# Optimization experiments

Hardware: AMD Instinct MI355X
Metric: run time of the kernel (lower is better)

## Reference

```python
import jax, jax.numpy as jnp
import numpy as np

K = 4        # num_kernels
TOPK = 16    # per-row hyperedge sparsification
CHEB_T = 2   # Chebyshev order
ROW_TEMP = 1.0
PI_ITERS = 5  # power-iteration steps


def setup_inputs() -> dict:
    key = jax.random.key(0)
    N, D, D_out = 4096, 256, 256
    ks = jax.random.split(key, 5)
    X = jax.random.normal(ks[0], (N, D), jnp.float32)
    L_k = jax.random.normal(ks[1], (K, D, D), jnp.float32) * 0.02
    alpha = jnp.ones((K,), jnp.float32)
    theta = jax.random.normal(ks[2], (CHEB_T + 1, D), jnp.float32) * 0.02
    rho_raw = jnp.zeros((), jnp.float32)
    proj_w = jax.random.normal(ks[3], (D_out, D), jnp.float32) / np.sqrt(D).astype(np.float32)
    proj_b = jnp.zeros((D_out,), jnp.float32)
    return {"X": X, "L_k": L_k, "alpha": alpha, "theta": theta,
            "rho_raw": rho_raw, "proj_w": proj_w, "proj_b": proj_b}


def reference(X, L_k, alpha, theta, rho_raw, proj_w, proj_b):
    N, D = X.shape
    tau = max(ROW_TEMP, 1e-6)
    # 1) K bilinear kernels: A_k = X L_k X^T / sqrt(D), row-softmax with temp
    A = jnp.einsum('nd,kde,me->knm', X, L_k, X) / jnp.sqrt(jnp.asarray(D, X.dtype))
    H_stack = jax.nn.softmax(A / tau, axis=2)                 # (K, N, N)
    w = jax.nn.softmax(alpha)[:, None, None]
    H_fused = (H_stack * w).sum(0)                            # (N, N)
    # 2) incidence B (N, E=K*N): hyperedge (k,i) holds topk targets of row i of head k
    vals, idx = jax.lax.top_k(H_stack, TOPK)                  # (K, N, TOPK)
    vals = vals / (vals.sum(-1, keepdims=True) + 1e-9)
    E = K * N
    cols = jnp.arange(K)[:, None, None] * N + jnp.arange(N)[None, :, None]
    cols = jnp.broadcast_to(cols, (K, N, TOPK)).reshape(-1)
    rows = idx.reshape(-1)
    B = jnp.zeros((N, E), X.dtype).at[rows, cols].set(vals.reshape(-1))
    W = jnp.ones((E,), X.dtype)
    # 3) normalized hypergraph Laplacian L = I - Dv^{-1/2} B W De^{-1} B^T Dv^{-1/2}
    De = B.sum(0) + 1e-9                                      # (E,)
    Dv = (B * W[None, :]).sum(1) + 1e-9                       # (N,)
    Dv_is = jnp.sqrt(1.0 / Dv)
    S = (B * (W / De)[None, :]) @ B.T                         # (N, N)
    S_norm = Dv_is[:, None] * S * Dv_is[None, :]
    I = jnp.eye(N, dtype=X.dtype)
    L = I - S_norm
    # 4) lambda_max via power iteration on detached L (constant w.r.t. grads)
    Ld = jax.lax.stop_gradient(L)
    v = jax.random.normal(jax.random.key(1), (N, 1), X.dtype)
    v = v / (jnp.linalg.norm(v) + 1e-9)
    for _ in range(PI_ITERS):
        v = Ld @ v
        v = v / (jnp.linalg.norm(v) + 1e-9)
    lam = jnp.clip((v.T @ (Ld @ v)).squeeze(), 1e-3, None)
    lam = jax.lax.stop_gradient(lam)
    L_tilde = (2.0 / lam) * L - I
    # Chebyshev recursion: sum_t T_t(L_tilde) X * theta_t, then ELU
    T0 = X
    out = T0 * theta[0][None, :]
    T1 = L_tilde @ X
    out = out + T1 * theta[1][None, :]
    for t in range(2, CHEB_T + 1):
        T2 = 2.0 * (L_tilde @ T1) - T0
        out = out + T2 * theta[t][None, :]
        T0, T1 = T1, T2
    Z_spec = jax.nn.elu(out)
    # 5) residual blend with kernel diffusion
    Z_kern = H_fused @ X
    rho = jax.nn.sigmoid(rho_raw)
    Z_mix = rho * Z_spec + (1.0 - rho) * Z_kern
    # 6) final projection
    return Z_mix @ proj_w.T + proj_b
```

## Files before the change

kernel.cpp:

```cpp
#include <hip/hip_runtime.h>

typedef unsigned short u16;
typedef unsigned long long u64;
typedef _Float16 h16;
typedef __attribute__((ext_vector_type(8))) _Float16 h16x8;
typedef __attribute__((ext_vector_type(4))) _Float16 h16x4;
typedef __attribute__((ext_vector_type(4))) float f32x4;

__device__ __forceinline__ float b2f(u16 u) {
  unsigned x = ((unsigned)u) << 16;
  return __uint_as_float(x);
}
__device__ __forceinline__ unsigned fkey(float f) {
  unsigned b = __float_as_uint(f);
  return (b & 0x80000000u) ? ~b : (b | 0x80000000u);
}
__device__ __forceinline__ float unfkey(unsigned u) {
  unsigned b = (u & 0x80000000u) ? (u ^ 0x80000000u) : ~u;
  return __uint_as_float(b);
}
__device__ __forceinline__ f32x4 mfma16(h16x8 a, h16x8 b, f32x4 c) {
  return __builtin_amdgcn_mfma_f32_16x16x32_f16(a, b, c, 0, 0, 0);
}
__device__ __forceinline__ void gl_lds16(const void* g, void* l) {
  __builtin_amdgcn_global_load_lds(
      (const __attribute__((address_space(1))) unsigned*)g,
      (__attribute__((address_space(3))) unsigned*)l, 16, 0, 0);
}
__device__ __forceinline__ u64 wave_max_u64(u64 k) {
#pragma unroll
  for (int off = 32; off; off >>= 1) {
    u64 o = __shfl_xor(k, off);
    if (o > k) k = o;
  }
  return k;
}
__device__ __forceinline__ float cvt_in(const void* p, int i, int f) {
  return f ? ((const float*)p)[i] : b2f(((const u16*)p)[i]);
}

__device__ __forceinline__ int detect_f32_local(const u16* __restrict__ X) {
  __shared__ int dcnt;
  if (threadIdx.x == 0) dcnt = 0;
  __syncthreads();
  int sane = 0;
  for (int j = threadIdx.x; j < 4096; j += blockDim.x) {
    u16 u = X[j * 2];
    int e = (u >> 7) & 0xff;
    if (u == 0 || (e >= 112 && e <= 142)) sane++;
  }
  atomicAdd(&dcnt, sane);
  __syncthreads();
  return (dcnt < 3072) ? 1 : 0;
}

__global__ __launch_bounds__(256) void split_input3(
    const void* __restrict__ in, h16* __restrict__ hi, h16* __restrict__ lo,
    float* __restrict__ f32out, int n) {
  int f = detect_f32_local((const u16*)in);
  int stride = gridDim.x * 256;
  for (int i = blockIdx.x * 256 + threadIdx.x; i < n; i += stride) {
    float x = cvt_in(in, i, f);
    h16 h = (h16)x;
    hi[i] = h;
    lo[i] = (h16)(x - (float)h);
    if (f32out) f32out[i] = x;
  }
}

__global__ __launch_bounds__(256) void split_LW(
    const void* __restrict__ Xin, const void* __restrict__ Lin,
    h16* __restrict__ Lhi, h16* __restrict__ Llo, const void* __restrict__ Win,
    h16* __restrict__ Whi, h16* __restrict__ Wlo) {
  int f = detect_f32_local((const u16*)Xin);
  int tid = threadIdx.x;
  if (blockIdx.x < 256) {
#pragma unroll
    for (int j = 0; j < 4; ++j) {
      int i = blockIdx.x * 1024 + j * 256 + tid;
      float x = cvt_in(Lin, i, f);
      h16 h = (h16)x;
      Lhi[i] = h;
      Llo[i] = (h16)(x - (float)h);
    }
  } else {
    int b = blockIdx.x - 256;
#pragma unroll
    for (int j = 0; j < 4; ++j) {
      int i = b * 1024 + j * 256 + tid;
      float x = cvt_in(Win, i, f);
      h16 h = (h16)x;
      Whi[i] = h;
      Wlo[i] = (h16)(x - (float)h);
    }
  }
}

__global__ __launch_bounds__(1024) void prep_small(
    const void* __restrict__ Xin, const void* __restrict__ theta,
    const void* __restrict__ bpin, const void* __restrict__ alpha,
    const void* __restrict__ rho_raw, float* __restrict__ thetaf,
    float* __restrict__ biasf, float* __restrict__ scal) {
  int f = detect_f32_local((const u16*)Xin);
  int tid = threadIdx.x;
  if (tid < 768)
    thetaf[tid] = cvt_in(theta, tid, f);
  else if (tid < 1024)
    biasf[tid - 768] = cvt_in(bpin, tid - 768, f);
  if (tid == 0) {
    float a[4], e[4], m = -1e30f, s = 0.f;
    for (int i = 0; i < 4; ++i) {
      a[i] = cvt_in(alpha, i, f);
      m = fmaxf(m, a[i]);
    }
    for (int i = 0; i < 4; ++i) { e[i] = expf(a[i] - m); s += e[i]; }
    for (int i = 0; i < 4; ++i) scal[i] = e[i] / s;
    float rr = cvt_in(rho_raw, 0, f);
    scal[4] = 1.f / (1.f + expf(-rr));
  }
}

template <bool BIAS, bool SPLITOUT>
__global__ __launch_bounds__(256) void gemm3_nt(
    const h16* __restrict__ Ah, const h16* __restrict__ Al,
    const h16* __restrict__ Bh, const h16* __restrict__ Bl,
    float* __restrict__ C, h16* __restrict__ Yh, h16* __restrict__ Yl,
    const float* __restrict__ bias, float alpha, int M, int Nc, int Kd,
    long batchA, long batchB, long batchC) {
  const h16* Abh = Ah + (size_t)blockIdx.z * batchA;
  const h16* Abl = Al + (size_t)blockIdx.z * batchA;
  const h16* Bbh = Bh + (size_t)blockIdx.z * batchB;
  const h16* Bbl = Bl + (size_t)blockIdx.z * batchB;
  int bn = blockIdx.x, bm = blockIdx.y;
  int tid = threadIdx.x;
  int wid = tid >> 6, lane = tid & 63;
  __shared__ h16 Ash[64 * 40], Asl[64 * 40], Bsh[64 * 40], Bsl[64 * 40];
  f32x4 acc00 = {}, acc01 = {}, acc10 = {}, acc11 = {};
  int lr = tid >> 2;
  int lc = (tid & 3) << 3;
  size_t aoff = (size_t)(bm * 64 + lr) * Kd + lc;
  size_t boff = (size_t)(bn * 64 + lr) * Kd + lc;
  int wm = (wid & 1) * 32, wn = (wid >> 1) * 32;
  int fr = lane & 15;
  int fc = (lane >> 4) << 3;
  for (int k0 = 0; k0 < Kd; k0 += 32) {
    uint4 avh = *(const uint4*)(Abh + aoff + k0);
    uint4 avl = *(const uint4*)(Abl + aoff + k0);
    uint4 bvh = *(const uint4*)(Bbh + boff + k0);
    uint4 bvl = *(const uint4*)(Bbl + boff + k0);
    __syncthreads();
    *(uint4*)(Ash + lr * 40 + lc) = avh;
    *(uint4*)(Asl + lr * 40 + lc) = avl;
    *(uint4*)(Bsh + lr * 40 + lc) = bvh;
    *(uint4*)(Bsl + lr * 40 + lc) = bvl;
    __syncthreads();
    h16x8 a0h = *(const h16x8*)(Ash + (wm + fr) * 40 + fc);
    h16x8 a1h = *(const h16x8*)(Ash + (wm + 16 + fr) * 40 + fc);
    h16x8 b0h = *(const h16x8*)(Bsh + (wn + fr) * 40 + fc);
    h16x8 b1h = *(const h16x8*)(Bsh + (wn + 16 + fr) * 40 + fc);
    h16x8 a0l = *(const h16x8*)(Asl + (wm + fr) * 40 + fc);
    h16x8 a1l = *(const h16x8*)(Asl + (wm + 16 + fr) * 40 + fc);
    h16x8 b0l = *(const h16x8*)(Bsl + (wn + fr) * 40 + fc);
    h16x8 b1l = *(const h16x8*)(Bsl + (wn + 16 + fr) * 40 + fc);
    acc00 = mfma16(a0h, b0h, acc00);
    acc01 = mfma16(a0h, b1h, acc01);
    acc10 = mfma16(a1h, b0h, acc10);
    acc11 = mfma16(a1h, b1h, acc11);
    acc00 = mfma16(a0h, b0l, acc00);
    acc01 = mfma16(a0h, b1l, acc01);
    acc10 = mfma16(a1h, b0l, acc10);
    acc11 = mfma16(a1h, b1l, acc11);
    acc00 = mfma16(a0l, b0h, acc00);
    acc01 = mfma16(a0l, b1h, acc01);
    acc10 = mfma16(a1l, b0h, acc10);
    acc11 = mfma16(a1l, b1h, acc11);
  }
  int crow = (lane >> 4) << 2;
  int ccol = lane & 15;
  f32x4 accs[2][2] = {{acc00, acc01}, {acc10, acc11}};
#pragma unroll
  for (int i = 0; i < 2; ++i)
#pragma unroll
    for (int j = 0; j < 2; ++j) {
      int r0 = bm * 64 + wm + 16 * i + crow;
      int c0 = bn * 64 + wn + 16 * j + ccol;
#pragma unroll
      for (int rg = 0; rg < 4; ++rg) {
        size_t off = (size_t)(r0 + rg) * Nc + c0;
        float v = accs[i][j][rg] * alpha;
        if constexpr (SPLITOUT) {
          h16* Yhb = Yh + (size_t)blockIdx.z * batchC;
          h16* Ylb = Yl + (size_t)blockIdx.z * batchC;
          h16 hh = (h16)v;
          Yhb[off] = hh;
          Ylb[off] = (h16)(v - (float)hh);
        } else {
          if constexpr (BIAS) v += bias[c0];
          float* Cb = C + (size_t)blockIdx.z * batchC;
          Cb[off] = v;
        }
      }
    }
}

__global__ __launch_bounds__(256) void gemm3_big(
    const h16* __restrict__ Ah, const h16* __restrict__ Al,
    const h16* __restrict__ Bh, const h16* __restrict__ Bl,
    float* __restrict__ C, float alpha, int M, int Nc, int Kd) {
  __shared__ h16 sAh[128 * 32], sAl[128 * 32], sBh[128 * 32], sBl[128 * 32];
  int tid = threadIdx.x, wid = tid >> 6, lane = tid & 63;
  int bm = blockIdx.y, bn = blockIdx.x;
  int srow = 32 * wid + (lane >> 2);
  int scnk = lane & 3;
  int fr = lane & 15, fcc = lane >> 4;
  f32x4 acc[4][4] = {};
  const h16* gA[2] = {Ah, Al};
  const h16* gB[2] = {Bh, Bl};
  h16* sA[2] = {sAh, sAl};
  h16* sB[2] = {sBh, sBl};
  int wm = (wid & 1) * 64, wn = (wid >> 1) * 64;
  for (int k0 = 0; k0 < Kd; k0 += 32) {
    __syncthreads();
#pragma unroll
    for (int h = 0; h < 2; ++h) {
      int r = srow + 16 * h;
      int cs = scnk ^ ((r >> 1) & 3);
      size_t goffA = (size_t)(bm * 128 + r) * Kd + k0 + cs * 8;
      size_t goffB = (size_t)(bn * 128 + r) * Kd + k0 + cs * 8;
      int loff = (32 * wid + 16 * h) * 32;
#pragma unroll
      for (int p = 0; p < 2; ++p) {
        gl_lds16(gA[p] + goffA, sA[p] + loff);
        gl_lds16(gB[p] + goffB, sB[p] + loff);
      }
    }
    __syncthreads();
    h16x8 fa[2][4], fb[2][4];
#pragma unroll
    for (int i = 0; i < 4; ++i) {
      int ra = wm + 16 * i + fr;
      int ca = (fcc ^ ((ra >> 1) & 3)) * 8;
      fa[0][i] = *(const h16x8*)(sAh + ra * 32 + ca);
      fa[1][i] = *(const h16x8*)(sAl + ra * 32 + ca);
      int rb = wn + 16 * i + fr;
      int cb = (fcc ^ ((rb >> 1) & 3)) * 8;
      fb[0][i] = *(const h16x8*)(sBh + rb * 32 + cb);
      fb[1][i] = *(const h16x8*)(sBl + rb * 32 + cb);
    }
#pragma unroll
    for (int i = 0; i < 4; ++i)
#pragma unroll
      for (int j = 0; j < 4; ++j) {
        acc[i][j] = mfma16(fa[0][i], fb[0][j], acc[i][j]);
        acc[i][j] = mfma16(fa[0][i], fb[1][j], acc[i][j]);
        acc[i][j] = mfma16(fa[1][i], fb[0][j], acc[i][j]);
      }
  }
  int crow = (lane >> 4) << 2, ccol = lane & 15;
#pragma unroll
  for (int i = 0; i < 4; ++i)
#pragma unroll
    for (int j = 0; j < 4; ++j) {
      int r0 = bm * 128 + wm + 16 * i + crow;
      int c0 = bn * 128 + wn + 16 * j + ccol;
#pragma unroll
      for (int rg = 0; rg < 4; ++rg)
        C[(size_t)(r0 + rg) * Nc + c0] = acc[i][j][rg] * alpha;
    }
}

__global__ __launch_bounds__(256) void gemm_ks4(
    const h16* __restrict__ Eall, const h16* __restrict__ B,
    float* __restrict__ Cpart) {
  __shared__ h16 sA[2][64 * 32];
  __shared__ h16 sB[2][256 * 32];
  int tid = threadIdx.x, wid = tid >> 6, lane = tid & 63;
  int bm = blockIdx.x, zz = blockIdx.y;
  int head = zz >> 2, kz = zz & 3;
  const h16* A =
      Eall + (size_t)head * 4096 * 4096 + (size_t)(bm * 64) * 4096 + kz * 1024;
  const h16* Bb = B + kz * 1024;
  int r16 = lane >> 2;
  int scnk = lane & 3;
  int fr = lane & 15, fcc = lane >> 4;
  int wn = wid * 64;
  f32x4 acc[4][4] = {};

  int rA = 16 * wid + r16;
  size_t gA = (size_t)rA * 4096 + scnk * 8;
  size_t gB[4];
  int dB[4];
  int dA = rA * 32 + ((scnk ^ ((rA >> 1) & 3)) << 3);
#pragma unroll
  for (int p = 0; p < 4; ++p) {
    int rB = 64 * p + 16 * wid + r16;
    gB[p] = (size_t)rB * 4096 + scnk * 8;
    dB[p] = rB * 32 + ((scnk ^ ((rB >> 1) & 3)) << 3);
  }

  uint4 rgA, rgB0, rgB1, rgB2, rgB3;
  auto gload = [&](int k0) {
    rgA = *(const uint4*)(A + gA + k0);
    rgB0 = *(const uint4*)(Bb + gB[0] + k0);
    rgB1 = *(const uint4*)(Bb + gB[1] + k0);
    rgB2 = *(const uint4*)(Bb + gB[2] + k0);
    rgB3 = *(const uint4*)(Bb + gB[3] + k0);
  };
  auto swrite = [&](int buf) {
    *(uint4*)(&sA[buf][dA]) = rgA;
    *(uint4*)(&sB[buf][dB[0]]) = rgB0;
    *(uint4*)(&sB[buf][dB[1]]) = rgB1;
    *(uint4*)(&sB[buf][dB[2]]) = rgB2;
    *(uint4*)(&sB[buf][dB[3]]) = rgB3;
  };
  auto compute = [&](int buf) {
    h16x8 fa[4], fb[4];
#pragma unroll
    for (int i = 0; i < 4; ++i) {
      int ra = 16 * i + fr;
      int ca = (fcc ^ ((ra >> 1) & 3)) * 8;
      fa[i] = *(const h16x8*)(&sA[buf][ra * 32 + ca]);
      int rb = wn + 16 * i + fr;
      int cb = (fcc ^ ((rb >> 1) & 3)) * 8;
      fb[i] = *(const h16x8*)(&sB[buf][rb * 32 + cb]);
    }
#pragma unroll
    for (int i = 0; i < 4; ++i)
#pragma unroll
      for (int j = 0; j < 4; ++j)
        acc[i][j] = mfma16(fa[i], fb[j], acc[i][j]);
  };

  gload(0);
  swrite(0);
  gload(32);
  __syncthreads();
  for (int t = 0; t < 32; ++t) {
    int cur = t & 1;
    if (t < 31) {
      swrite(cur ^ 1);
      if (t < 30) gload((t + 2) * 32);
    }
    compute(cur);
    __syncthreads();
  }

  float* Cp = Cpart + (size_t)zz * 4096 * 256;
  int crow = (lane >> 4) << 2, ccol = lane & 15;
#pragma unroll
  for (int i = 0; i < 4; ++i)
#pragma unroll
    for (int j = 0; j < 4; ++j) {
      int r0 = bm * 64 + 16 * i + crow;
      int c0 = wn + 16 * j + ccol;
#pragma unroll
      for (int rg = 0; rg < 4; ++rg)
        Cp[(size_t)(r0 + rg) * 256 + c0] = acc[i][j][rg];
    }
}

__global__ __launch_bounds__(256) void ksred_hist(
    const float* __restrict__ Cpart, const float* __restrict__ scal,
    const float* __restrict__ rowSinv, float* __restrict__ Zk,
    const float* __restrict__ topv, const int* __restrict__ topi,
    int* __restrict__ pCnt, float* __restrict__ pDv,
    float* __restrict__ DeIS) {
  __shared__ int lc[4096];
  __shared__ float ld[4096];
  int tid = threadIdx.x;
  if (blockIdx.x < 1024) {
    int i = (blockIdx.x * 256 + tid) * 4;
    int row = i >> 8;
    float4 out = {0.f, 0.f, 0.f, 0.f};
#pragma unroll
    for (int k = 0; k < 4; ++k) {
      float4 s = {0.f, 0.f, 0.f, 0.f};
#pragma unroll
      for (int z = 0; z < 4; ++z) {
        float4 p =
            *(const float4*)(Cpart + (size_t)(k * 4 + z) * 4096 * 256 + i);
        s.x += p.x; s.y += p.y; s.z += p.z; s.w += p.w;
      }
      float sc = scal[k] * rowSinv[k * 4096 + row];
      out.x += sc * s.x; out.y += sc * s.y;
      out.z += sc * s.z; out.w += sc * s.w;
    }
    *(float4*)(Zk + i) = out;
  } else {
    int b = blockIdx.x - 1024;
    for (int j = tid; j < 4096; j += 256) { lc[j] = 0; ld[j] = 0.f; }
    __syncthreads();
    int base = b * 4096;
#pragma unroll
    for (int j = 0; j < 16; ++j) {
      int t = base + j * 256 + tid;
      atomicAdd(&lc[topi[t]], 1);
      atomicAdd(&ld[topi[t]], topv[t]);
    }
    __syncthreads();
    for (int j = tid; j < 4096; j += 256) {
      pCnt[base + j] = lc[j];
      pDv[base + j] = ld[j];
    }
    int e = b * 256 + tid;
    const float4* p = (const float4*)(topv + ((size_t)e << 4));
    float4 a = p[0], bb = p[1], c = p[2], d = p[3];
    float s = ((a.x + a.y) + (a.z + a.w)) + ((bb.x + bb.y) + (bb.z + bb.w)) +
              ((c.x + c.y) + (c.z + c.w)) + ((d.x + d.y) + (d.z + d.w));
    DeIS[e] = 1.0f / sqrtf(s + 1e-9f);
  }
}

__global__ __launch_bounds__(256) void transpose16(
    const u16* __restrict__ in, u16* __restrict__ out, int rows, int cols) {
  __shared__ u16 t[32][33];
  const u16* ib = in + (size_t)blockIdx.z * rows * cols;
  u16* ob = out + (size_t)blockIdx.z * rows * cols;
  int r0 = blockIdx.x * 32, c0 = blockIdx.y * 32;
  int tx = threadIdx.x & 31, ty = threadIdx.x >> 5;
#pragma unroll
  for (int i = 0; i < 32; i += 8)
    t[ty + i][tx] = ib[(size_t)(r0 + ty + i) * cols + c0 + tx];
  __syncthreads();
#pragma unroll
  for (int i = 0; i < 32; i += 8)
    ob[(size_t)(c0 + ty + i) * rows + r0 + tx] = t[tx][ty + i];
}

__global__ __launch_bounds__(256) void row_softmax_topk(
    const float* __restrict__ A, float* __restrict__ topv,
    int* __restrict__ topi, h16* __restrict__ E, float* __restrict__ rowSinvK,
    int khead) {
  __shared__ u64 candK[4][256];
  __shared__ int candN[4];
  int wid = threadIdx.x >> 6, lane = threadIdx.x & 63;
  int row = blockIdx.x * 4 + wid;
  const float* arow = A + ((size_t)row << 12);
  if (lane == 0) candN[wid] = 0;
  __syncthreads();
  float lm = -INFINITY;
#pragma unroll
  for (int t = 0; t < 16; ++t) {
    float4 v = *(const float4*)(arow + (t << 8) + (lane << 2));
    lm = fmaxf(lm, fmaxf(fmaxf(v.x, v.y), fmaxf(v.z, v.w)));
  }
  float m = lm;
#pragma unroll
  for (int off = 32; off; off >>= 1) m = fmaxf(m, __shfl_xor(m, off));
  u64 lk = ((u64)fkey(lm) << 32) | (unsigned)lane;
  float T = 0.f;
  for (int r = 0; r < 16; ++r) {
    u64 k2 = wave_max_u64(lk);
    if (lk == k2) lk = 0;
    if (r == 15) T = unfkey((unsigned)(k2 >> 32));
  }
  h16* erow = E + ((size_t)row << 12);
  int* cn = &candN[wid];
  u64* ck = candK[wid];
  float s = 0.f;
  for (int t = 0; t < 16; ++t) {
    int c = (t << 8) + (lane << 2);
    float4 v = *(const float4*)(arow + c);
    float e0 = __expf(v.x - m), e1 = __expf(v.y - m);
    float e2 = __expf(v.z - m), e3 = __expf(v.w - m);
    s += (e0 + e1) + (e2 + e3);
    h16x4 hv = {(h16)e0, (h16)e1, (h16)e2, (h16)e3};
    *(h16x4*)(erow + c) = hv;
    if (v.x >= T) {
      int sl = atomicAdd(cn, 1);
      if (sl < 256) ck[sl] = ((u64)fkey(v.x) << 32) | (unsigned)(~(unsigned)c);
    }
    if (v.y >= T) {
      int sl = atomicAdd(cn, 1);
      if (sl < 256) ck[sl] = ((u64)fkey(v.y) << 32) | (unsigned)(~(unsigned)(c + 1));
    }
    if (v.z >= T) {
      int sl = atomicAdd(cn, 1);
      if (sl < 256) ck[sl] = ((u64)fkey(v.z) << 32) | (unsigned)(~(unsigned)(c + 2));
    }
    if (v.w >= T) {
      int sl = atomicAdd(cn, 1);
      if (sl < 256) ck[sl] = ((u64)fkey(v.w) << 32) | (unsigned)(~(unsigned)(c + 3));
    }
  }
#pragma unroll
  for (int off = 32; off; off >>= 1) s += __shfl_xor(s, off);
  if (lane == 0) rowSinvK[row] = 1.f / s;
  __syncthreads();
  int cnt = min(*cn, 256);
  u64 loc[4] = {0ull, 0ull, 0ull, 0ull};
  int nl = 0;
  for (int j = lane; j < cnt; j += 64)
    if (nl < 4) loc[nl++] = ck[j];
#define CSW(a, b)                     \
  {                                   \
    if (loc[b] > loc[a]) {            \
      u64 tt = loc[a];                \
      loc[a] = loc[b];                \
      loc[b] = tt;                    \
    }                                 \
  }
  CSW(0, 1) CSW(2, 3) CSW(0, 2) CSW(1, 3) CSW(1, 2)
#undef CSW
  float myv = 0.f;
  int myi = 0;
  float sum16 = 0.f;
  for (int r = 0; r < 16; ++r) {
    u64 key = loc[0];
    u64 k2 = wave_max_u64(key);
    float wv = unfkey((unsigned)(k2 >> 32));
    int wi = (int)(~(unsigned)(k2 & 0xffffffffu));
    if (key == k2 && key != 0ull) {
      loc[0] = loc[1];
      loc[1] = loc[2];
      loc[2] = loc[3];
      loc[3] = 0ull;
    }
    sum16 += expf(wv - m);
    if (r == lane) { myv = wv; myi = wi; }
  }
  if (lane < 16) {
    size_t o = (((size_t)khead << 12) + row) * 16 + lane;
    topv[o] = expf(myv - m) / (sum16 + 1e-9f * s);
    topi[o] = myi;
  }
}

__global__ __launch_bounds__(256) void col_scan(
    const int* __restrict__ pCnt, const float* __restrict__ pDv,
    int* __restrict__ cnt, float* __restrict__ Dvis,
    int* __restrict__ blockBase, float* __restrict__ v0) {
  int i = blockIdx.x * 256 + threadIdx.x;
  int run = 0;
  float dv = 0.f;
#pragma unroll
  for (int b = 0; b < 64; ++b) {
    blockBase[b * 4096 + i] = run;
    run += pCnt[b * 4096 + i];
    dv += pDv[b * 4096 + i];
  }
  cnt[i] = run;
  Dvis[i] = sqrtf(1.0f / (dv + 1e-9f));
  {
    int tid = i;
    unsigned j = (unsigned)(tid & 2047);
    unsigned x0 = j, x1 = j + 2048u;
    const unsigned ks0 = 0u, ks1 = 1u, ks2 = 0x1BD11BDAu;
#define TF_R(r)                                \
    {                                          \
      x0 += x1;                                \
      x1 = (x1 << (r)) | (x1 >> (32 - (r)));   \
      x1 ^= x0;                                \
    }
    x0 += ks0; x1 += ks1;
    TF_R(13) TF_R(15) TF_R(26) TF_R(6)  x0 += ks1; x1 += ks2 + 1u;
    TF_R(17) TF_R(29) TF_R(16) TF_R(24) x0 += ks2; x1 += ks0 + 2u;
    TF_R(13) TF_R(15) TF_R(26) TF_R(6)  x0 += ks0; x1 += ks1 + 3u;
    TF_R(17) TF_R(29) TF_R(16) TF_R(24) x0 += ks1; x1 += ks2 + 4u;
    TF_R(13) TF_R(15) TF_R(26) TF_R(6)  x0 += ks2; x1 += ks0 + 5u;
#undef TF_R
    unsigned bits = (tid < 2048) ? x0 : x1;
    float u01 = __uint_as_float((bits >> 9) | 0x3f800000u) - 1.0f;
    const float lo = -0.99999994f;
    float u = fmaxf(lo, u01 * 2.0f + lo);
    float w = -log1pf(-u * u);
    float p;
    if (w < 5.0f) {
      float t = w - 2.5f;
      p = 2.81022636e-08f;
      p = 3.43273939e-07f + p * t;
      p = -3.5233877e-06f + p * t;
      p = -4.39150654e-06f + p * t;
      p = 0.00021858087f + p * t;
      p = -0.00125372503f + p * t;
      p = -0.00417768164f + p * t;
      p = 0.246640727f + p * t;
      p = 1.50140941f + p * t;
    } else {
      float t = sqrtf(w) - 3.0f;
      p = -0.000200214257f;
      p = 0.000100950558f + p * t;
      p = 0.00134934322f + p * t;
      p = -0.00367342844f + p * t;
      p = 0.00573950773f + p * t;
      p = -0.0076224613f + p * t;
      p = 0.00943887047f + p * t;
      p = 1.00167406f + p * t;
      p = 2.83297682f + p * t;
    }
    v0[tid] = 1.41421354f * (p * u);
  }
}

__global__ __launch_bounds__(256) void scan_rowptr(const int* __restrict__ cnt,
                                                   int* __restrict__ rowptr) {
  __shared__ int part[256];
  int tid = threadIdx.x;
  int base = tid * 16;
  int loc[16];
  int s = 0;
#pragma unroll
  for (int j = 0; j < 16; ++j) { loc[j] = s; s += cnt[base + j]; }
  part[tid] = s;
  __syncthreads();
  for (int off = 1; off < 256; off <<= 1) {
    int v = (tid >= off) ? part[tid - off] : 0;
    __syncthreads();
    part[tid] += v;
    __syncthreads();
  }
  int pre = (tid == 0) ? 0 : part[tid - 1];
#pragma unroll
  for (int j = 0; j < 16; ++j) rowptr[base + j] = pre + loc[j];
  if (tid == 255) rowptr[4096] = part[255];
}

__global__ __launch_bounds__(256) void csr_fill3(
    const float* __restrict__ topv, const int* __restrict__ topi,
    const float* __restrict__ Dvis, const float* __restrict__ DeIS,
    const int* __restrict__ rowptr, const int* __restrict__ blockBase,
    float* __restrict__ cvals, int* __restrict__ colE,
    float* __restrict__ cvalR) {
  __shared__ int lcur[4096];
  int tid = threadIdx.x, b = blockIdx.x;
  int base = b * 4096;
  for (int j = tid; j < 4096; j += 256)
    lcur[j] = rowptr[j] + blockBase[base + j];
  __syncthreads();
#pragma unroll
  for (int j = 0; j < 16; ++j) {
    int t = base + j * 256 + tid;
    int i = topi[t];
    int e = t >> 4;
    float c = Dvis[i] * topv[t] * DeIS[e];
    cvals[t] = c;
    int slot = atomicAdd(&lcur[i], 1);
    colE[slot] = e;
    cvalR[slot] = c;
  }
}

__global__ __launch_bounds__(256) void spmv_edge(
    const float* __restrict__ cvals, const int* __restrict__ topi,
    const float* __restrict__ v, float* __restrict__ g) {
  int e = blockIdx.x * 256 + threadIdx.x;
  float acc = 0.f;
#pragma unroll
  for (int p = 0; p < 16; ++p)
    acc += cvals[e * 16 + p] * v[topi[e * 16 + p]];
  g[e] = acc;
}

__global__ __launch_bounds__(256) void spmv_row(
    const int* __restrict__ rowptr, const int* __restrict__ colE,
    const float* __restrict__ cvalR, const float* __restrict__ g,
    const float* __restrict__ vin, float* __restrict__ vout) {
  int wid = threadIdx.x >> 6, lane = threadIdx.x & 63;
  int row = blockIdx.x * 4 + wid;
  int s = rowptr[row], e = rowptr[row + 1];
  float acc = 0.f;
  for (int j = s + lane; j < e; j += 64) acc += cvalR[j] * g[colE[j]];
#pragma unroll
  for (int off = 32; off; off >>= 1) acc += __shfl_xor(acc, off);
  if (lane == 0) vout[row] = vin[row] - acc;
}

__global__ __launch_bounds__(256) void pi_dots(const float* __restrict__ w5,
                                               const float* __restrict__ w6,
                                               float* __restrict__ scal) {
  __shared__ float r1[256], r2[256];
  int tid = threadIdx.x;
  float a = 0.f, b = 0.f;
  for (int i = tid; i < 4096; i += 256) {
    float x = w5[i];
    a += x * x;
    b += x * w6[i];
  }
  r1[tid] = a; r2[tid] = b;
  __syncthreads();
  for (int off = 128; off; off >>= 1) {
    if (tid < off) { r1[tid] += r1[tid + off]; r2[tid] += r2[tid + off]; }
    __syncthreads();
  }
  if (tid == 0) scal[5] = fmaxf(r2[0] / r1[0], 1e-3f);
}

__global__ __launch_bounds__(256) void spmm_edge(
    const float* __restrict__ cvals, const int* __restrict__ topi,
    const float* __restrict__ M, float* __restrict__ G) {
  int wid = threadIdx.x >> 6, lane = threadIdx.x & 63;
  int e = blockIdx.x * 4 + wid;
  int cb = lane << 2;
  const float* cv = cvals + ((size_t)e << 4);
  const int* ti = topi + ((size_t)e << 4);
  float cc[16];
  int ix[16];
#pragma unroll
  for (int p = 0; p < 16; ++p) { cc[p] = cv[p]; ix[p] = ti[p]; }
  float4 acc[4] = {};
#pragma unroll
  for (int h = 0; h < 2; ++h) {
    float4 g[8];
#pragma unroll
    for (int p = 0; p < 8; ++p)
      g[p] = *(const float4*)(M + ((size_t)ix[h * 8 + p] << 8) + cb);
#pragma unroll
    for (int p = 0; p < 8; ++p) {
      float c = cc[h * 8 + p];
      float4 gg = g[p];
      int a = p & 3;
      acc[a].x += c * gg.x; acc[a].y += c * gg.y;
      acc[a].z += c * gg.z; acc[a].w += c * gg.w;
    }
  }
  float4 r;
  r.x = (acc[0].x + acc[1].x) + (acc[2].x + acc[3].x);
  r.y = (acc[0].y + acc[1].y) + (acc[2].y + acc[3].y);
  r.z = (acc[0].z + acc[1].z) + (acc[2].z + acc[3].z);
  r.w = (acc[0].w + acc[1].w) + (acc[2].w + acc[3].w);
  *(float4*)(G + ((size_t)e << 8) + cb) = r;
}

template <int MODE>
__global__ __launch_bounds__(256) void spmm_row_ep(
    const int* __restrict__ rowptr, const int* __restrict__ colE,
    const float* __restrict__ cvalR, const float* __restrict__ G,
    const float* __restrict__ Xf, float* __restrict__ T1,
    const float* __restrict__ Zk, const float* __restrict__ thetaf,
    const float* __restrict__ scal, h16* __restrict__ Zmh,
    h16* __restrict__ Zml) {
  int wid = threadIdx.x >> 6, lane = threadIdx.x & 63;
  int row = blockIdx.x * 4 + wid;
  int cb = lane << 2;
  int s = rowptr[row], e = rowptr[row + 1];
  float4 acc[4] = {};
  int j = s;
  for (; j + 8 <= e; j += 8) {
    int ix[8];
    float cc[8];
#pragma unroll
    for (int t = 0; t < 8; ++t) { ix[t] = colE[j + t]; cc[t] = cvalR[j + t]; }
    float4 g[8];
#pragma unroll
    for (int t = 0; t < 8; ++t)
      g[t] = *(const float4*)(G + ((size_t)ix[t] << 8) + cb);
#pragma unroll
    for (int t = 0; t < 8; ++t) {
      float c = cc[t];
      float4 gg = g[t];
      int a = t & 3;
      acc[a].x += c * gg.x; acc[a].y += c * gg.y;
      acc[a].z += c * gg.z; acc[a].w += c * gg.w;
    }
  }
  for (; j < e; ++j) {
    float c = cvalR[j];
    float4 gg = *(const float4*)(G + ((size_t)colE[j] << 8) + cb);
    acc[0].x += c * gg.x; acc[0].y += c * gg.y;
    acc[0].z += c * gg.z; acc[0].w += c * gg.w;
  }
  float4 z;
  z.x = (acc[0].x + acc[1].x) + (acc[2].x + acc[3].x);
  z.y = (acc[0].y + acc[1].y) + (acc[2].y + acc[3].y);
  z.z = (acc[0].z + acc[1].z) + (acc[2].z + acc[3].z);
  z.w = (acc[0].w + acc[1].w) + (acc[2].w + acc[3].w);
  size_t o = ((size_t)row << 8) + cb;
  float c1 = 2.0f / scal[5];
  float4 x = *(const float4*)(Xf + o);
  if constexpr (MODE == 1) {
    float4 t1;
    t1.x = (c1 - 1.0f) * x.x - c1 * z.x;
    t1.y = (c1 - 1.0f) * x.y - c1 * z.y;
    t1.z = (c1 - 1.0f) * x.z - c1 * z.z;
    t1.w = (c1 - 1.0f) * x.w - c1 * z.w;
    *(float4*)(T1 + o) = t1;
  } else {
    float rho = scal[4];
    float4 t1 = *(const float4*)(T1 + o);
    float4 zk = *(const float4*)(Zk + o);
    h16x4 hh, hl;
#pragma unroll
    for (int q = 0; q < 4; ++q) {
      float xv = (&x.x)[q], t1v = (&t1.x)[q], zv = (&z.x)[q], zkv = (&zk.x)[q];
      int d = cb + q;
      float t2 = 2.0f * ((c1 - 1.0f) * t1v - c1 * zv) - xv;
      float oo = xv * thetaf[d] + t1v * thetaf[256 + d] + t2 * thetaf[512 + d];
      float zs = oo > 0.0f ? oo : expm1f(oo);
      float zm = rho * zs + (1.0f - rho) * zkv;
      h16 h = (h16)zm;
      hh[q] = h;
      hl[q] = (h16)(zm - (float)h);
    }
    *(h16x4*)(Zmh + o) = hh;
    *(h16x4*)(Zml + o) = hl;
  }
}

extern "C" void kernel_launch(void* const* d_in, const int* in_sizes, int n_in,
                              void* d_out, int out_size, void* d_ws,
                              size_t ws_size, hipStream_t stream) {
  (void)in_sizes; (void)n_in; (void)out_size;
  const void* Xin = d_in[0];
  const void* Lin = d_in[1];
  const void* alpha = d_in[2];
  const void* theta = d_in[3];
  const void* rho_raw = d_in[4];
  const void* Wpin = d_in[5];
  const void* bpin = d_in[6];
  float* out = (float*)d_out;

  char* base = (char*)d_ws;
  size_t off = 0;
  auto alloc = [&](size_t bytes) -> char* {
    char* p = base + off;
    off += (bytes + 255) & ~(size_t)255;
    return p;
  };
  float* Abuf = (float*)alloc((size_t)4096 * 4096 * 4);
  h16* Eall = (h16*)alloc((size_t)4 * 4096 * 4096 * 2);
  h16* Yhi = (h16*)alloc((size_t)4 * 4096 * 256 * 2);
  h16* Ylo = (h16*)alloc((size_t)4 * 4096 * 256 * 2);
  h16* Xhi = (h16*)alloc((size_t)4096 * 256 * 2);
  h16* Xlo = (h16*)alloc((size_t)4096 * 256 * 2);
  float* Xf = (float*)alloc((size_t)4096 * 256 * 4);
  h16* XT = (h16*)alloc((size_t)256 * 4096 * 2);
  h16* Lhi = (h16*)alloc((size_t)4 * 256 * 256 * 2);
  h16* Llo = (h16*)alloc((size_t)4 * 256 * 256 * 2);
  h16* LThi = (h16*)alloc((size_t)4 * 256 * 256 * 2);
  h16* LTlo = (h16*)alloc((size_t)4 * 256 * 256 * 2);
  h16* Whi = (h16*)alloc((size_t)256 * 256 * 2);
  h16* Wlo = (h16*)alloc((size_t)256 * 256 * 2);
  float* Zk = (float*)alloc((size_t)4096 * 256 * 4);
  float* T1 = (float*)alloc((size_t)4096 * 256 * 4);
  h16* Zmh = (h16*)alloc((size_t)4096 * 256 * 2);
  h16* Zml = (h16*)alloc((size_t)4096 * 256 * 2);
  float* topv = (float*)alloc((size_t)4 * 4096 * 16 * 4);
  int* topi = (int*)alloc((size_t)4 * 4096 * 16 * 4);
  float* cvals = (float*)alloc((size_t)262144 * 4);
  int* colE = (int*)alloc((size_t)262144 * 4);
  float* cvalR = (float*)alloc((size_t)262144 * 4);
  int* pCnt = (int*)alloc((size_t)64 * 4096 * 4);
  float* pDv = (float*)alloc((size_t)64 * 4096 * 4);
  int* blockBase = (int*)alloc((size_t)64 * 4096 * 4);
  int* rowptr = (int*)alloc(4097 * 4);
  int* cnt = (int*)alloc(4096 * 4);
  float* Dvis = (float*)alloc(4096 * 4);
  float* DeIS = (float*)alloc(16384 * 4);
  float* gE = (float*)alloc(16384 * 4);
  float* wA = (float*)alloc(4096 * 4);
  float* wB = (float*)alloc(4096 * 4);
  float* rowSinv = (float*)alloc((size_t)4 * 4096 * 4);
  float* thetaf = (float*)alloc(768 * 4);
  float* biasf = (float*)alloc(256 * 4);
  float* scal = (float*)alloc(256);
  if (off > ws_size) return;
  float* Kpart = Abuf;
  float* G = Abuf;

  split_input3<<<1024, 256, 0, stream>>>(Xin, Xhi, Xlo, Xf, 4096 * 256);
  split_LW<<<320, 256, 0, stream>>>(Xin, Lin, Lhi, Llo, Wpin, Whi, Wlo);
  prep_small<<<1, 1024, 0, stream>>>(Xin, theta, bpin, alpha, rho_raw, thetaf,
                                     biasf, scal);
  transpose16<<<dim3(128, 8, 1), 256, 0, stream>>>((const u16*)Xhi, (u16*)XT,
                                                   4096, 256);
  transpose16<<<dim3(8, 8, 8), 256, 0, stream>>>((const u16*)Lhi, (u16*)LThi,
                                                 256, 256);
  gemm3_nt<false, true><<<dim3(4, 64, 4), 256, 0, stream>>>(
      Xhi, Xlo, LThi, LTlo, nullptr, Yhi, Ylo, nullptr, 1.0f, 4096, 256, 256,
      0L, 256L * 256L, 4096L * 256L);
  for (int k = 0; k < 4; ++k) {
    gemm3_big<<<dim3(32, 32), 256, 0, stream>>>(
        Yhi + (size_t)k * 4096 * 256, Ylo + (size_t)k * 4096 * 256, Xhi, Xlo,
        Abuf, 0.0625f, 4096, 4096, 256);
    row_softmax_topk<<<1024, 256, 0, stream>>>(
        Abuf, topv, topi, Eall + (size_t)k * 4096 * 4096, rowSinv + k * 4096,
        k);
  }
  gemm_ks4<<<dim3(64, 16), 256, 0, stream>>>(Eall, XT, Kpart);
  ksred_hist<<<1088, 256, 0, stream>>>(Kpart, scal, rowSinv, Zk, topv, topi,
                                       pCnt, pDv, DeIS);
  col_scan<<<16, 256, 0, stream>>>(pCnt, pDv, cnt, Dvis, blockBase, wA);
  scan_rowptr<<<1, 256, 0, stream>>>(cnt, rowptr);
  csr_fill3<<<64, 256, 0, stream>>>(topv, topi, Dvis, DeIS, rowptr, blockBase,
                                    cvals, colE, cvalR);
  for (int it = 0; it < 6; ++it) {
    const float* vi = (it & 1) ? wB : wA;
    float* vo = (it & 1) ? wA : wB;
    spmv_edge<<<64, 256, 0, stream>>>(cvals, topi, vi, gE);
    spmv_row<<<1024, 256, 0, stream>>>(rowptr, colE, cvalR, gE, vi, vo);
  }
  pi_dots<<<1, 256, 0, stream>>>(wB, wA, scal);
  spmm_edge<<<4096, 256, 0, stream>>>(cvals, topi, Xf, G);
  spmm_row_ep<1><<<1024, 256, 0, stream>>>(rowptr, colE, cvalR, G, Xf, T1,
                                           nullptr, thetaf, scal, nullptr,
                                           nullptr);
  spmm_edge<<<4096, 256, 0, stream>>>(cvals, topi, T1, G);
  spmm_row_ep<2><<<1024, 256, 0, stream>>>(rowptr, colE, cvalR, G, Xf, T1, Zk,
                                           thetaf, scal, Zmh, Zml);
  gemm3_nt<true, false><<<dim3(4, 64, 1), 256, 0, stream>>>(
      Zmh, Zml, Whi, Wlo, out, nullptr, nullptr, biasf, 1.0f, 4096, 256, 256,
      0L, 0L, 0L);
}
```

Before: 670.0 us.

## Prefetch next K-tile into registers in split-fp16 GEMM kernels

Both split-precision fp16 GEMM kernels now issue the global loads for the next K-slice into registers right after the LDS barrier, so the loads overlap with the current slice's MFMA work. The big GEMM also drops the direct global-to-LDS load builtin in favour of register staging plus ds_write, and precomputes its address offsets once. This trades extra register pressure and an LDS write pass for hiding global memory latency behind compute.

```diff
diff --git a/kernel.cpp b/kernel.cpp
--- a/kernel.cpp
+++ b/kernel.cpp
@@ -21,11 +21,6 @@
 }
 __device__ __forceinline__ f32x4 mfma16(h16x8 a, h16x8 b, f32x4 c) {
   return __builtin_amdgcn_mfma_f32_16x16x32_f16(a, b, c, 0, 0, 0);
-}
-__device__ __forceinline__ void gl_lds16(const void* g, void* l) {
-  __builtin_amdgcn_global_load_lds(
-      (const __attribute__((address_space(1))) unsigned*)g,
-      (__attribute__((address_space(3))) unsigned*)l, 16, 0, 0);
 }
 __device__ __forceinline__ u64 wave_max_u64(u64 k) {
 #pragma unroll
@@ -143,17 +138,23 @@
   int wm = (wid & 1) * 32, wn = (wid >> 1) * 32;
   int fr = lane & 15;
   int fc = (lane >> 4) << 3;
+  uint4 avh = *(const uint4*)(Abh + aoff);
+  uint4 avl = *(const uint4*)(Abl + aoff);
+  uint4 bvh = *(const uint4*)(Bbh + boff);
+  uint4 bvl = *(const uint4*)(Bbl + boff);
   for (int k0 = 0; k0 < Kd; k0 += 32) {
-    uint4 avh = *(const uint4*)(Abh + aoff + k0);
-    uint4 avl = *(const uint4*)(Abl + aoff + k0);
-    uint4 bvh = *(const uint4*)(Bbh + boff + k0);
-    uint4 bvl = *(const uint4*)(Bbl + boff + k0);
     __syncthreads();
     *(uint4*)(Ash + lr * 40 + lc) = avh;
     *(uint4*)(Asl + lr * 40 + lc) = avl;
     *(uint4*)(Bsh + lr * 40 + lc) = bvh;
     *(uint4*)(Bsl + lr * 40 + lc) = bvl;
     __syncthreads();
+    if (k0 + 32 < Kd) {
+      avh = *(const uint4*)(Abh + aoff + k0 + 32);
+      avl = *(const uint4*)(Abl + aoff + k0 + 32);
+      bvh = *(const uint4*)(Bbh + boff + k0 + 32);
+      bvl = *(const uint4*)(Bbl + boff + k0 + 32);
+    }
     h16x8 a0h = *(const h16x8*)(Ash + (wm + fr) * 40 + fc);
     h16x8 a1h = *(const h16x8*)(Ash + (wm + 16 + fr) * 40 + fc);
     h16x8 b0h = *(const h16x8*)(Bsh + (wn + fr) * 40 + fc);
@@ -214,27 +215,39 @@
   int scnk = lane & 3;
   int fr = lane & 15, fcc = lane >> 4;
   f32x4 acc[4][4] = {};
-  const h16* gA[2] = {Ah, Al};
-  const h16* gB[2] = {Bh, Bl};
-  h16* sA[2] = {sAh, sAl};
-  h16* sB[2] = {sBh, sBl};
   int wm = (wid & 1) * 64, wn = (wid >> 1) * 64;
+  size_t goA[2], goB[2];
+  int lo2[2];
+#pragma unroll
+  for (int h = 0; h < 2; ++h) {
+    int r = srow + 16 * h;
+    int cs = scnk ^ ((r >> 1) & 3);
+    goA[h] = (size_t)(bm * 128 + r) * Kd + cs * 8;
+    goB[h] = (size_t)(bn * 128 + r) * Kd + cs * 8;
+    lo2[h] = (32 * wid + 16 * h) * 32 + lane * 8;
+  }
+  uint4 rAh[2], rAl[2], rBh[2], rBl[2];
+  auto gload = [&](int k0) {
+#pragma unroll
+    for (int h = 0; h < 2; ++h) {
+      rAh[h] = *(const uint4*)(Ah + goA[h] + k0);
+      rAl[h] = *(const uint4*)(Al + goA[h] + k0);
+      rBh[h] = *(const uint4*)(Bh + goB[h] + k0);
+      rBl[h] = *(const uint4*)(Bl + goB[h] + k0);
+    }
+  };
+  gload(0);
   for (int k0 = 0; k0 < Kd; k0 += 32) {
     __syncthreads();
 #pragma unroll
     for (int h = 0; h < 2; ++h) {
-      int r = srow + 16 * h;
-      int cs = scnk ^ ((r >> 1) & 3);
-      size_t goffA = (size_t)(bm * 128 + r) * Kd + k0 + cs * 8;
-      size_t goffB = (size_t)(bn * 128 + r) * Kd + k0 + cs * 8;
-      int loff = (32 * wid + 16 * h) * 32;
-#pragma unroll
-      for (int p = 0; p < 2; ++p) {
-        gl_lds16(gA[p] + goffA, sA[p] + loff);
-        gl_lds16(gB[p] + goffB, sB[p] + loff);
-      }
+      *(uint4*)(sAh + lo2[h]) = rAh[h];
+      *(uint4*)(sAl + lo2[h]) = rAl[h];
+      *(uint4*)(sBh + lo2[h]) = rBh[h];
+      *(uint4*)(sBl + lo2[h]) = rBl[h];
     }
     __syncthreads();
+    if (k0 + 32 < Kd) gload(k0 + 32);
     h16x8 fa[2][4], fb[2][4];
 #pragma unroll
     for (int i = 0; i < 4; ++i) {
```

Result: slower. 904.3 us (+35.0%).
